# Kernel optimization log

Measured on AMD Instinct MI355X. Metric: run time of the kernel, lower is better.

Reference implementation:

```python
import jax, jax.numpy as jnp
import numpy as np

_J6 = jnp.array([[0,0,0,0,0,1],[0,0,0,0,-1,0],[0,0,0,1,0,0],
                 [0,0,1,0,0,0],[0,-1,0,0,0,0],[1,0,0,0,0,0]], dtype=jnp.float32)
_PAIRS4 = [(0,1),(0,2),(0,3),(1,2),(1,3),(2,3)]
H = 16  # n_heads

def _ln(x, g, b, eps=1e-5):
    m = jnp.mean(x, axis=-1, keepdims=True)
    v = jnp.var(x, axis=-1, keepdims=True)
    return (x - m) / jnp.sqrt(v + eps) * g + b

def _exterior(p1, p2):
    # Plucker coordinates of the line through p1,p2 in R^4 -> R^6, normalized
    parts = [p1[..., i] * p2[..., j] - p1[..., j] * p2[..., i] for i, j in _PAIRS4]
    L = jnp.stack(parts, axis=-1)
    n = jnp.linalg.norm(L, axis=-1, keepdims=True)
    return L / jnp.maximum(n, 1e-12)

def _iterated_gram_attn(x, Wqkv, bqkv, W1w, W2w, W1r, W2r, Wmv, bmv, Wmg, bmg,
                        mem_scale, iter_mix, decay_logits, Wout, bout):
    B, T, D = x.shape
    dh = D // H
    # ---- standard causal attention branch ----
    qkv = (x @ Wqkv + bqkv).reshape(B, T, 3, H, dh)
    q = jnp.transpose(qkv[:, :, 0], (0, 2, 1, 3))  # bhtd
    k = jnp.transpose(qkv[:, :, 1], (0, 2, 1, 3))
    v = jnp.transpose(qkv[:, :, 2], (0, 2, 1, 3))
    scores = jnp.einsum('bhtd,bhsd->bhts', q, k) * (dh ** -0.5)
    causal = jnp.tril(jnp.ones((T, T), dtype=bool))
    scores = jnp.where(causal, scores, -jnp.inf)
    attn = jax.nn.softmax(scores, axis=-1)  # dropout is eval-mode identity
    seq_out = jnp.einsum('bhts,bhsd->bhtd', attn, v).transpose(0, 2, 1, 3).reshape(B, T, D)
    # ---- Gram memory branch ----
    x_prev = jnp.concatenate([jnp.zeros_like(x[:, :1]), x[:, :-1]], axis=1)
    w1 = (x_prev @ W1w).reshape(B, T, H, 4)
    w2 = (x @ W2w).reshape(B, T, H, 4)
    write_lines = _exterior(w1, w2)                       # (B,T,H,6)
    r1 = (x @ W1r).reshape(B, T, H, 4)
    r2 = (x @ W2r).reshape(B, T, H, 4)
    read_lines = _exterior(r1, r2)                        # (B,T,H,6)
    Jw = jnp.einsum('bthi,ij->bhtj', write_lines, _J6)    # (B,H,T,6)
    rd = jnp.transpose(read_lines, (0, 2, 1, 3))          # (B,H,T,6)
    decays = jax.nn.sigmoid(decay_logits)                 # (H,)
    pos = jnp.arange(T, dtype=x.dtype)
    outer = Jw[..., :, None] * Jw[..., None, :]           # (B,H,T,6,6)
    dinv = (1.0 / jnp.maximum(decays, 1e-6))[:, None] ** pos[None, :]  # (H,T)
    M = jnp.cumsum(outer * dinv[None, :, :, None, None], axis=2)
    M = jnp.concatenate([jnp.zeros_like(M[:, :, :1]), M[:, :, :-1]], axis=2)  # shift: strictly past
    dfwd = decays[:, None] ** pos[None, :]
    M = M * dfwd[None, :, :, None, None]                  # (B,H,T,6,6)
    rdM = jnp.einsum('bhti,bhtij->bhtj', rd, M)
    score_M = jnp.sum(rdM * rd, axis=-1)                  # (B,H,T)
    score_M2 = jnp.sum(rdM * rdM, axis=-1)
    alpha = jax.nn.sigmoid(iter_mix[0])
    mem_score = (1 - alpha) * score_M + alpha * score_M2
    mem_val = x @ Wmv + bmv                               # (B,T,D)
    gate = jax.nn.sigmoid(x @ Wmg + bmg)                  # (B,T,H)
    gated = jax.nn.sigmoid(jnp.transpose(mem_score, (0, 2, 1)) * mem_scale[None, None, :]) * gate
    gated = jnp.mean(gated, axis=-1, keepdims=True)       # (B,T,1)
    return (seq_out + gated * mem_val) @ Wout + bout

def _block(x, ln1_g, ln1_b, Wqkv, bqkv, W1w, W2w, W1r, W2r, Wmv, bmv, Wmg, bmg,
           mem_scale, iter_mix, decay_logits, Wout, bout,
           ln2_g, ln2_b, Wfc, bfc, Wproj, bproj):
    h = _ln(x, ln1_g, ln1_b)
    x = x + _iterated_gram_attn(h, Wqkv, bqkv, W1w, W2w, W1r, W2r, Wmv, bmv,
                                Wmg, bmg, mem_scale, iter_mix, decay_logits, Wout, bout)
    h2 = _ln(x, ln2_g, ln2_b)
    mlp = jax.nn.gelu(h2 @ Wfc + bfc, approximate=False) @ Wproj + bproj
    return x + mlp

def setup_inputs() -> dict:
    key = jax.random.key(0)
    B, T, D = 2, 1024, 1024
    dff = 4 * D
    ks = jax.random.split(key, 16)
    s = 0.02
    inp = {
        'x': jax.random.normal(ks[0], (B, T, D), jnp.float32),
        'ln1_g': jnp.ones((D,), jnp.float32), 'ln1_b': jnp.zeros((D,), jnp.float32),
        'Wqkv': jax.random.normal(ks[1], (D, 3 * D), jnp.float32) * s,
        'bqkv': jnp.zeros((3 * D,), jnp.float32),
        'W1w': jax.random.normal(ks[2], (D, 4 * H), jnp.float32) * s,
        'W2w': jax.random.normal(ks[3], (D, 4 * H), jnp.float32) * s,
        'W1r': jax.random.normal(ks[4], (D, 4 * H), jnp.float32) * s,
        'W2r': jax.random.normal(ks[5], (D, 4 * H), jnp.float32) * s,
        'Wmv': jax.random.normal(ks[6], (D, D), jnp.float32) * s,
        'bmv': jnp.zeros((D,), jnp.float32),
        'Wmg': jax.random.normal(ks[7], (D, H), jnp.float32) * s,
        'bmg': jnp.zeros((H,), jnp.float32),
        'mem_scale': jnp.full((H,), 0.1, jnp.float32),
        'iter_mix': jnp.zeros((1,), jnp.float32),
        'decay_logits': jnp.full((H,), 4.6, jnp.float32) + 0.1 * jax.random.normal(ks[8], (H,), jnp.float32),
        'Wout': jax.random.normal(ks[9], (D, D), jnp.float32) * s,
        'bout': jnp.zeros((D,), jnp.float32),
        'ln2_g': jnp.ones((D,), jnp.float32), 'ln2_b': jnp.zeros((D,), jnp.float32),
        'Wfc': jax.random.normal(ks[10], (D, dff), jnp.float32) * s,
        'bfc': jnp.zeros((dff,), jnp.float32),
        'Wproj': jax.random.normal(ks[11], (dff, D), jnp.float32) * s,
        'bproj': jnp.zeros((D,), jnp.float32),
    }
    return inp

def reference(x, ln1_g, ln1_b, Wqkv, bqkv, W1w, W2w, W1r, W2r, Wmv, bmv, Wmg, bmg,
              mem_scale, iter_mix, decay_logits, Wout, bout,
              ln2_g, ln2_b, Wfc, bfc, Wproj, bproj):
    return _block(x, ln1_g, ln1_b, Wqkv, bqkv, W1w, W2w, W1r, W2r, Wmv, bmv, Wmg, bmg,
                  mem_scale, iter_mix, decay_logits, Wout, bout,
                  ln2_g, ln2_b, Wfc, bfc, Wproj, bproj)
```

## Files before the change

### kernel.cpp

```cpp
#include <hip/hip_runtime.h>
#include <hip/hip_bf16.h>
#include <math.h>

typedef float f32x4 __attribute__((ext_vector_type(4)));
typedef _Float16 f16x8 __attribute__((ext_vector_type(8)));
typedef _Float16 f16x4 __attribute__((ext_vector_type(4)));

#define TT 1024
#define DD 1024
#define QS 4608

typedef __attribute__((address_space(1))) const void gas_void;
typedef __attribute__((address_space(3))) void las_void;
static __device__ __forceinline__ void gl_lds16(const void* g, void* l) {
  __builtin_amdgcn_global_load_lds((gas_void*)g, (las_void*)l, 16, 0, 0);
}

__global__ __launch_bounds__(512) void gemm_t16(
    const _Float16* __restrict__ A, const _Float16* __restrict__ Wt,
    const float* __restrict__ bias, void* __restrict__ Cv,
    int N, int K, int act, int gx, int mode, int ktiles) {
  __shared__ __align__(16) _Float16 As[3][128 * 32];
  __shared__ __align__(16) _Float16 Bs[3][128 * 32];
  const int tid = threadIdx.x;
  const int lane = tid & 63;
  const int wid = tid >> 6;
  const int wr = wid >> 1, wc = wid & 1;
  const int g = lane >> 4, l16 = lane & 15;
  const int cpx = gridDim.x >> 3;
  const int wg = (blockIdx.x & 7) * cpx + (blockIdx.x >> 3);
  const int row0 = (wg / gx) * 128, col0 = (wg % gx) * 128;
  const int kbeg = blockIdx.y * ktiles * 32;

  f32x4 acc[2][4];
#pragma unroll
  for (int m = 0; m < 2; ++m)
#pragma unroll
    for (int n = 0; n < 4; ++n) acc[m][n] = (f32x4){0.f, 0.f, 0.f, 0.f};

  const int srow = tid >> 2;
  const int goff = ((tid & 3) ^ ((srow >> 1) & 3)) << 3;
  const _Float16* agp = A + (size_t)(row0 + srow) * K + kbeg + goff;
  const _Float16* bgp = Wt + (size_t)(col0 + srow) * K + kbeg + goff;
  const int ldst = tid * 16;

  const int prm = (l16 >> 1) & 3;

  gl_lds16(agp, (char*)As[0] + ldst);
  gl_lds16(bgp, (char*)Bs[0] + ldst);
  if (1 < ktiles) {
    gl_lds16(agp + 32, (char*)As[1] + ldst);
    gl_lds16(bgp + 32, (char*)Bs[1] + ldst);
  }

  int cs = 0, ss = 2;
  for (int kt = 0; kt < ktiles; ++kt) {
    if (kt < ktiles - 1) asm volatile("s_waitcnt vmcnt(2)" ::: "memory");
    else                 asm volatile("s_waitcnt vmcnt(0)" ::: "memory");
    __builtin_amdgcn_s_barrier();
    __builtin_amdgcn_sched_barrier(0);
    if (kt + 2 < ktiles) {
      const int kp = (kt + 2) * 32;
      gl_lds16(agp + kp, (char*)As[ss] + ldst);
      gl_lds16(bgp + kp, (char*)Bs[ss] + ldst);
    }
    f16x8 af[2], bf[4];
#pragma unroll
    for (int m = 0; m < 2; ++m) {
      const int r = wr * 32 + m * 16 + l16;
      af[m] = *(const f16x8*)(As[cs] + r * 32 + ((g ^ prm) << 3));
    }
#pragma unroll
    for (int n = 0; n < 4; ++n) {
      const int r = wc * 64 + n * 16 + l16;
      bf[n] = *(const f16x8*)(Bs[cs] + r * 32 + ((g ^ prm) << 3));
    }
#pragma unroll
    for (int m = 0; m < 2; ++m)
#pragma unroll
      for (int n = 0; n < 4; ++n)
        acc[m][n] = __builtin_amdgcn_mfma_f32_16x16x32_f16(af[m], bf[n], acc[m][n], 0, 0, 0);
    cs = (cs == 2) ? 0 : cs + 1;
    ss = (ss == 2) ? 0 : ss + 1;
  }
#pragma unroll
  for (int m = 0; m < 2; ++m) {
#pragma unroll
    for (int n = 0; n < 4; ++n) {
      const int col = col0 + wc * 64 + n * 16 + l16;
      const float bv = (mode != 2 && bias) ? bias[col] : 0.f;
#pragma unroll
      for (int rg = 0; rg < 4; ++rg) {
        const int row = row0 + wr * 32 + m * 16 + g * 4 + rg;
        const size_t off = (size_t)row * N + col;
        float v = acc[m][n][rg] + bv;
        if (act == 1) v = 0.5f * v * (1.f + erff(v * 0.70710678118654752f));
        if (mode == 2) atomicAdd(&((float*)Cv)[off], v);
        else ((_Float16*)Cv)[off] = (_Float16)v;
      }
    }
  }
}

__global__ __launch_bounds__(256) void transT(const float* __restrict__ W,
                                              _Float16* __restrict__ WT, int K, int N) {
  __shared__ float tile[64][65];
  const int n0 = blockIdx.x * 64, k0 = blockIdx.y * 64;
  const int tn = threadIdx.x & 63, tk4 = threadIdx.x >> 6;
#pragma unroll
  for (int it = 0; it < 16; ++it) {
    const int k = k0 + it * 4 + tk4;
    tile[tn][it * 4 + tk4] = W[(size_t)k * N + n0 + tn];
  }
  __syncthreads();
  const int on = threadIdx.x >> 2, ok = threadIdx.x & 3;
  f16x8 a, b;
#pragma unroll
  for (int j = 0; j < 8; ++j) {
    a[j] = (_Float16)tile[on][ok * 16 + j];
    b[j] = (_Float16)tile[on][ok * 16 + 8 + j];
  }
  _Float16* dst = WT + (size_t)(n0 + on) * K + k0 + ok * 16;
  *(f16x8*)dst = a;
  *(f16x8*)(dst + 8) = b;
}

__global__ __launch_bounds__(256) void prep_megaT(
    const float* __restrict__ Wqkv, const float* __restrict__ W1w, const float* __restrict__ W2w,
    const float* __restrict__ W1r, const float* __restrict__ W2r, const float* __restrict__ Wmg,
    const float* __restrict__ Wmv, _Float16* __restrict__ WmT) {
  __shared__ float tile[64][65];
  const int n0 = blockIdx.x * 64, k0 = blockIdx.y * 64;
  const int tn = threadIdx.x & 63, tk4 = threadIdx.x >> 6;
#pragma unroll
  for (int it = 0; it < 16; ++it) {
    const int k = k0 + it * 4 + tk4;
    const int n = n0 + tn;
    float v;
    if (n < 3072) v = Wqkv[(size_t)k * 3072 + n];
    else if (n < 3136) v = W1w[k * 64 + n - 3072];
    else if (n < 3200) v = W2w[k * 64 + n - 3136];
    else if (n < 3264) v = W1r[k * 64 + n - 3200];
    else if (n < 3328) v = W2r[k * 64 + n - 3264];
    else if (n < 3344) v = Wmg[k * 16 + n - 3328];
    else if (n < 3584) v = 0.f;
    else v = Wmv[(size_t)k * 1024 + n - 3584];
    tile[tn][it * 4 + tk4] = v;
  }
  __syncthreads();
  const int on = threadIdx.x >> 2, ok = threadIdx.x & 3;
  f16x8 a, b;
#pragma unroll
  for (int j = 0; j < 8; ++j) {
    a[j] = (_Float16)tile[on][ok * 16 + j];
    b[j] = (_Float16)tile[on][ok * 16 + 8 + j];
  }
  _Float16* dst = WmT + (size_t)(n0 + on) * 1024 + k0 + ok * 16;
  *(f16x8*)dst = a;
  *(f16x8*)(dst + 8) = b;
}

__global__ void bm_init(const float* __restrict__ bqkv, const float* __restrict__ bmg,
                        const float* __restrict__ bmv, float* __restrict__ bm) {
  const int col = blockIdx.x * 256 + threadIdx.x;
  if (col >= 4608) return;
  float b = 0.f;
  if (col < 3072) b = bqkv[col];
  else if (col >= 3328 && col < 3344) b = bmg[col - 3328];
  else if (col >= 3584) b = bmv[col - 3584];
  bm[col] = b;
}

__global__ __launch_bounds__(256) void ln16(const float* __restrict__ in,
    const float* __restrict__ gw, const float* __restrict__ bw, _Float16* __restrict__ out) {
  const int row = blockIdx.x, tid = threadIdx.x;
  const float* x = in + (size_t)row * DD;
  const float4 v = *(const float4*)(x + tid * 4);
  float s = v.x + v.y + v.z + v.w;
  float sq = v.x * v.x + v.y * v.y + v.z * v.z + v.w * v.w;
#pragma unroll
  for (int off = 32; off >= 1; off >>= 1) { s += __shfl_xor(s, off); sq += __shfl_xor(sq, off); }
  __shared__ float red[8];
  const int lane = tid & 63, wv = tid >> 6;
  if (lane == 0) { red[wv] = s; red[4 + wv] = sq; }
  __syncthreads();
  s = red[0] + red[1] + red[2] + red[3];
  sq = red[4] + red[5] + red[6] + red[7];
  const float mean = s * (1.f / 1024.f);
  const float var = sq * (1.f / 1024.f) - mean * mean;
  const float rstd = rsqrtf(var + 1e-5f);
  const float4 g4 = *(const float4*)(gw + tid * 4);
  const float4 b4 = *(const float4*)(bw + tid * 4);
  f16x4 o;
  o[0] = (_Float16)((v.x - mean) * rstd * g4.x + b4.x);
  o[1] = (_Float16)((v.y - mean) * rstd * g4.y + b4.y);
  o[2] = (_Float16)((v.z - mean) * rstd * g4.z + b4.z);
  o[3] = (_Float16)((v.w - mean) * rstd * g4.w + b4.w);
  *(f16x4*)(out + (size_t)row * DD + tid * 4) = o;
}

static __device__ __forceinline__ int swzA(int row, int k) {
  return row * 64 + ((((k >> 3) ^ row) & 7) << 3) + (k & 7);
}
static __device__ __forceinline__ int swzV(int row, int k) {
  return row * 64 + ((((k >> 3) ^ row ^ (row >> 3)) & 7) << 3) + (k & 7);
}

__global__ __launch_bounds__(256) void attn_mfma(const _Float16* __restrict__ qkv,
                                                 _Float16* __restrict__ seq_out) {
  __shared__ __align__(16) _Float16 Kl[64 * 64];
  __shared__ __align__(16) _Float16 Vt[64 * 64];
  __shared__ __align__(16) _Float16 Pl[4][16 * 64];
  const int tid = threadIdx.x, lane = tid & 63, wq = tid >> 6;
  const int g = lane >> 4, l16 = lane & 15;
  const int qt = blockIdx.x, hh = blockIdx.y, bb = blockIdx.z;
  const int nt = qt + 1;

  f16x8 qf[2];
  {
    const _Float16* qp = qkv + (size_t)(bb * TT + qt * 64 + wq * 16 + l16) * QS + hh * 64;
#pragma unroll
    for (int ks = 0; ks < 2; ++ks) {
      const f16x8 a = *(const f16x8*)(qp + ks * 32 + g * 8);
#pragma unroll
      for (int j = 0; j < 8; ++j) qf[ks][j] = (_Float16)((float)a[j] * 0.125f);
    }
  }

  f32x4 oacc[4];
#pragma unroll
  for (int n = 0; n < 4; ++n) oacc[n] = (f32x4){0.f, 0.f, 0.f, 0.f};
  float m[4] = {-INFINITY, -INFINITY, -INFINITY, -INFINITY};
  float l[4] = {0.f, 0.f, 0.f, 0.f};

  const int skey = tid >> 2, sc4 = tid & 3;

  for (int tt = 0; tt < nt; ++tt) {
    if (tt) __syncthreads();
    {
      const _Float16* kp = qkv + (size_t)(bb * TT + tt * 64 + skey) * QS + hh * 64 + 1024;
      const _Float16* vp = kp + 1024;
#pragma unroll
      for (int ii = 0; ii < 4; ++ii) {
        const int d0 = sc4 * 4 + ii * 16;
        *(f16x4*)(Kl + swzA(skey, d0)) = *(const f16x4*)(kp + d0);
        const f16x4 vv = *(const f16x4*)(vp + d0);
        Vt[swzV(d0 + 0, skey)] = vv[0];
        Vt[swzV(d0 + 1, skey)] = vv[1];
        Vt[swzV(d0 + 2, skey)] = vv[2];
        Vt[swzV(d0 + 3, skey)] = vv[3];
      }
    }
    __syncthreads();
    f32x4 s[4];
#pragma unroll
    for (int n = 0; n < 4; ++n) s[n] = (f32x4){0.f, 0.f, 0.f, 0.f};
#pragma unroll
    for (int ks = 0; ks < 2; ++ks) {
      f16x8 kf[4];
#pragma unroll
      for (int n = 0; n < 4; ++n) kf[n] = *(const f16x8*)(Kl + swzA(n * 16 + l16, ks * 32 + g * 8));
#pragma unroll
      for (int n = 0; n < 4; ++n)
        s[n] = __builtin_amdgcn_mfma_f32_16x16x32_f16(qf[ks], kf[n], s[n], 0, 0, 0);
    }
    if (tt == qt) {
      const int rloc = wq * 16 + g * 4;
#pragma unroll
      for (int n = 0; n < 4; ++n) {
        const int cloc = n * 16 + l16;
#pragma unroll
        for (int reg = 0; reg < 4; ++reg)
          if (cloc > rloc + reg) s[n][reg] = -INFINITY;
      }
    }
    float f[4];
#pragma unroll
    for (int reg = 0; reg < 4; ++reg) {
      float t = fmaxf(fmaxf(s[0][reg], s[1][reg]), fmaxf(s[2][reg], s[3][reg]));
#pragma unroll
      for (int off = 1; off < 16; off <<= 1) t = fmaxf(t, __shfl_xor(t, off));
      const float nm = fmaxf(m[reg], t);
      f[reg] = __expf(m[reg] - nm);
      m[reg] = nm;
    }
    float rs[4] = {0.f, 0.f, 0.f, 0.f};
#pragma unroll
    for (int n = 0; n < 4; ++n) {
#pragma unroll
      for (int reg = 0; reg < 4; ++reg) {
        const float p = __expf(s[n][reg] - m[reg]);
        rs[reg] += p;
        Pl[wq][swzA(g * 4 + reg, n * 16 + l16)] = (_Float16)p;
      }
    }
#pragma unroll
    for (int reg = 0; reg < 4; ++reg) {
      float t = rs[reg];
#pragma unroll
      for (int off = 1; off < 16; off <<= 1) t += __shfl_xor(t, off);
      l[reg] = l[reg] * f[reg] + t;
    }
#pragma unroll
    for (int n = 0; n < 4; ++n)
#pragma unroll
      for (int reg = 0; reg < 4; ++reg) oacc[n][reg] *= f[reg];
#pragma unroll
    for (int ks = 0; ks < 2; ++ks) {
      const f16x8 pa = *(const f16x8*)(Pl[wq] + swzA(l16, ks * 32 + g * 8));
      f16x8 vb[4];
#pragma unroll
      for (int n = 0; n < 4; ++n) vb[n] = *(const f16x8*)(Vt + swzV(n * 16 + l16, ks * 32 + g * 8));
#pragma unroll
      for (int n = 0; n < 4; ++n)
        oacc[n] = __builtin_amdgcn_mfma_f32_16x16x32_f16(pa, vb[n], oacc[n], 0, 0, 0);
    }
  }
#pragma unroll
  for (int n = 0; n < 4; ++n) {
#pragma unroll
    for (int reg = 0; reg < 4; ++reg) {
      const int r = qt * 64 + wq * 16 + g * 4 + reg;
      seq_out[(size_t)(bb * TT + r) * DD + hh * 64 + n * 16 + l16] = (_Float16)(oacc[n][reg] / l[reg]);
    }
  }
}

static __device__ __forceinline__ void ext6(const float* a, const float* b, float* L) {
  L[0] = a[0] * b[1] - a[1] * b[0];
  L[1] = a[0] * b[2] - a[2] * b[0];
  L[2] = a[0] * b[3] - a[3] * b[0];
  L[3] = a[1] * b[2] - a[2] * b[1];
  L[4] = a[1] * b[3] - a[3] * b[1];
  L[5] = a[2] * b[3] - a[3] * b[2];
  const float n = sqrtf(L[0]*L[0] + L[1]*L[1] + L[2]*L[2] + L[3]*L[3] + L[4]*L[4] + L[5]*L[5]);
  const float s = 1.f / fmaxf(n, 1e-12f);
#pragma unroll
  for (int i = 0; i < 6; ++i) L[i] *= s;
}

__global__ void lines_post(const _Float16* __restrict__ mega, float* __restrict__ jw,
                           float* __restrict__ rdv, float* __restrict__ gate) {
  const int idx = blockIdx.x * 256 + threadIdx.x;
  const int h = idx & 15;
  const int bt = idx >> 4;
  const int t = bt & 1023;
  const int b = bt >> 10;
  const _Float16* row = mega + (size_t)bt * QS + 3072;
  float w1[4] = {0.f, 0.f, 0.f, 0.f}, w2[4], r1[4], r2[4];
  if (t > 0) {
#pragma unroll
    for (int i = 0; i < 4; ++i) w1[i] = (float)row[-QS + h * 4 + i];
  }
#pragma unroll
  for (int i = 0; i < 4; ++i) {
    w2[i] = (float)row[64 + h * 4 + i];
    r1[i] = (float)row[128 + h * 4 + i];
    r2[i] = (float)row[192 + h * 4 + i];
  }
  const float gp = (float)row[256 + h];
  float wl[6], rl[6];
  ext6(w1, w2, wl);
  ext6(r1, r2, rl);
  const size_t o = ((size_t)(b * 16 + h) * 1024 + t) * 6;
  jw[o + 0] =  wl[5]; jw[o + 1] = -wl[4]; jw[o + 2] =  wl[3];
  jw[o + 3] =  wl[2]; jw[o + 4] = -wl[1]; jw[o + 5] =  wl[0];
#pragma unroll
  for (int i = 0; i < 6; ++i) rdv[o + i] = rl[i];
  gate[idx] = 1.f / (1.f + __expf(-gp));
}

static __device__ __forceinline__ int midx(int i, int j) {
  return (i <= j) ? (i * (13 - i)) / 2 + (j - i) : (j * (13 - j)) / 2 + (i - j);
}

__global__ __launch_bounds__(64) void gram_scan(const float* __restrict__ jwv,
    const float* __restrict__ rdv, const float* __restrict__ decay_logits,
    const float* __restrict__ iter_mix, float* __restrict__ mem_score) {
  const int h = blockIdx.x & 15, b = blockIdx.x >> 4;
  const int lane = threadIdx.x;
  const float decay = 1.f / (1.f + __expf(-decay_logits[h]));
  const float alpha = 1.f / (1.f + __expf(-iter_mix[0]));
  __shared__ float sd[64 * 193];
  const size_t base = (size_t)(b * 16 + h) * 1024 * 6;
  for (int it = 0; it < 96; ++it) {
    const int idx = it * 64 + lane;
    const int t = idx / 6, i = idx - 6 * t;
    const int ld = t >> 4, s = t & 15;
    sd[ld * 193 + s * 6 + i] = jwv[base + idx];
    sd[ld * 193 + 96 + s * 6 + i] = rdv[base + idx];
  }
  __syncthreads();
  const float* seg = sd + lane * 193;

  float C[21];
#pragma unroll
  for (int e = 0; e < 21; ++e) C[e] = 0.f;
  for (int s = 0; s < 16; ++s) {
    float J[6], dJ[6];
#pragma unroll
    for (int i = 0; i < 6; ++i) { J[i] = seg[s * 6 + i]; dJ[i] = decay * J[i]; }
#pragma unroll
    for (int i = 0; i < 6; ++i)
#pragma unroll
      for (int j = i; j < 6; ++j)
        C[midx(i, j)] = decay * C[midx(i, j)] + dJ[i] * J[j];
  }
  const float d2 = decay * decay, d4 = d2 * d2, d8 = d4 * d4;
  float fk = d8 * d8;
#pragma unroll
  for (int k = 0; k < 6; ++k) {
    const int off = 1 << k;
#pragma unroll
    for (int e = 0; e < 21; ++e) {
      const float u = __shfl(C[e], lane - off);
      if (lane >= off) C[e] += fk * u;
    }
    fk = fk * fk;
  }
  float M[21];
#pragma unroll
  for (int e = 0; e < 21; ++e) {
    const float u = __shfl(C[e], lane - 1);
    M[e] = (lane >= 1) ? u : 0.f;
  }
  float* msp = mem_score + (size_t)(b * 16 + h) * 1024 + lane * 16;
  for (int s = 0; s < 16; ++s) {
    float J[6], r[6];
#pragma unroll
    for (int i = 0; i < 6; ++i) { J[i] = seg[s * 6 + i]; r[i] = seg[96 + s * 6 + i]; }
    float rdM[6];
#pragma unroll
    for (int i = 0; i < 6; ++i) {
      float a = 0.f;
#pragma unroll
      for (int j = 0; j < 6; ++j) a += M[midx(i, j)] * r[j];
      rdM[i] = a;
    }
    float s1 = 0.f, s2 = 0.f;
#pragma unroll
    for (int i = 0; i < 6; ++i) { s1 += rdM[i] * r[i]; s2 += rdM[i] * rdM[i]; }
    msp[s] = (1.f - alpha) * s1 + alpha * s2;
    float dJ[6];
#pragma unroll
    for (int i = 0; i < 6; ++i) dJ[i] = decay * J[i];
#pragma unroll
    for (int i = 0; i < 6; ++i)
#pragma unroll
      for (int j = i; j < 6; ++j)
        M[midx(i, j)] = decay * M[midx(i, j)] + dJ[i] * J[j];
  }
}

__global__ __launch_bounds__(256) void combine_kernel(const _Float16* __restrict__ seq,
    const _Float16* __restrict__ mega, const float* __restrict__ ms,
    const float* __restrict__ gate, const float* __restrict__ mem_scale,
    _Float16* __restrict__ outp) {
  const int bt = blockIdx.x;
  const int b = bt >> 10, t = bt & 1023;
  __shared__ float hterm[16];
  const int tid = threadIdx.x;
  if (tid < 16) {
    const float sc = ms[(size_t)(b * 16 + tid) * 1024 + t];
    const float gt = gate[(size_t)bt * 16 + tid];
    hterm[tid] = (1.f / (1.f + __expf(-sc * mem_scale[tid]))) * gt;
  }
  __syncthreads();
  float acc = 0.f;
#pragma unroll
  for (int h = 0; h < 16; ++h) acc += hterm[h];
  const float g = acc * (1.f / 16.f);
  const f16x4 s4 = *(const f16x4*)(seq + (size_t)bt * 1024 + tid * 4);
  const f16x4 m4 = *(const f16x4*)(mega + (size_t)bt * QS + 3584 + tid * 4);
  f16x4 o;
#pragma unroll
  for (int j = 0; j < 4; ++j) o[j] = (_Float16)((float)s4[j] + g * (float)m4[j]);
  *(f16x4*)(outp + (size_t)bt * 1024 + tid * 4) = o;
}

__global__ void addb_init(const float* __restrict__ src, const float* __restrict__ bias,
                          float* __restrict__ dst) {
  const size_t i = (size_t)blockIdx.x * 256 + threadIdx.x;
  const int c4 = (int)(i & 255);
  const float4 s = ((const float4*)src)[i];
  const float4 b = ((const float4*)bias)[c4];
  float4 o;
  o.x = s.x + b.x; o.y = s.y + b.y; o.z = s.z + b.z; o.w = s.w + b.w;
  ((float4*)dst)[i] = o;
}

extern "C" void kernel_launch(void* const* d_in, const int* in_sizes, int n_in,
                              void* d_out, int out_size, void* d_ws, size_t ws_size,
                              hipStream_t stream) {
  (void)in_sizes; (void)n_in; (void)out_size; (void)ws_size;
  const float* x       = (const float*)d_in[0];
  const float* ln1_g   = (const float*)d_in[1];
  const float* ln1_b   = (const float*)d_in[2];
  const float* Wqkv    = (const float*)d_in[3];
  const float* bqkv    = (const float*)d_in[4];
  const float* W1w     = (const float*)d_in[5];
  const float* W2w     = (const float*)d_in[6];
  const float* W1r     = (const float*)d_in[7];
  const float* W2r     = (const float*)d_in[8];
  const float* Wmv     = (const float*)d_in[9];
  const float* bmv     = (const float*)d_in[10];
  const float* Wmg     = (const float*)d_in[11];
  const float* bmg     = (const float*)d_in[12];
  const float* mscale  = (const float*)d_in[13];
  const float* itermix = (const float*)d_in[14];
  const float* dlogits = (const float*)d_in[15];
  const float* Wout    = (const float*)d_in[16];
  const float* bout    = (const float*)d_in[17];
  const float* ln2_g   = (const float*)d_in[18];
  const float* ln2_b   = (const float*)d_in[19];
  const float* Wfc     = (const float*)d_in[20];
  const float* bfc     = (const float*)d_in[21];
  const float* Wproj   = (const float*)d_in[22];
  const float* bproj   = (const float*)d_in[23];
  float* out = (float*)d_out;
  float* ws = (float*)d_ws;

  const size_t M1 = 1u << 20;
  _Float16* h16    = (_Float16*)ws;
  _Float16* WmT    = (_Float16*)(ws + 1 * M1);
  float*    bm     = ws + 3407872;
  float*    jw     = ws + 3538944;
  float*    rd     = ws + 3538944 + 196608;
  float*    gate   = ws + 3538944 + 393216;
  float*    ms     = ws + 3538944 + 425984;
  float*    y      = ws + 4 * M1;
  _Float16* mega   = (_Float16*)(ws + 6 * M1);
  _Float16* fc16   = (_Float16*)(ws + 6 * M1);
  _Float16* seq16  = (_Float16*)(ws + 11010048);
  _Float16* WoutT  = (_Float16*)(ws + 12058624);
  _Float16* WfcT   = (_Float16*)(ws + 12 * M1);
  _Float16* WprojT = (_Float16*)(ws + 14 * M1);

  prep_megaT<<<dim3(72, 16), 256, 0, stream>>>(Wqkv, W1w, W2w, W1r, W2r, Wmg, Wmv, WmT);
  bm_init<<<18, 256, 0, stream>>>(bqkv, bmg, bmv, bm);
  transT<<<dim3(16, 16), 256, 0, stream>>>(Wout, WoutT, 1024, 1024);
  transT<<<dim3(64, 16), 256, 0, stream>>>(Wfc, WfcT, 1024, 4096);
  transT<<<dim3(16, 64), 256, 0, stream>>>(Wproj, WprojT, 4096, 1024);

  ln16<<<2048, 256, 0, stream>>>(x, ln1_g, ln1_b, h16);
  gemm_t16<<<576, 512, 0, stream>>>(h16, WmT, bm, mega, 4608, 1024, 0, 36, 1, 32);
  attn_mfma<<<dim3(16, 16, 2), 256, 0, stream>>>(mega, seq16);
  lines_post<<<128, 256, 0, stream>>>(mega, jw, rd, gate);
  gram_scan<<<32, 64, 0, stream>>>(jw, rd, dlogits, itermix, ms);
  combine_kernel<<<2048, 256, 0, stream>>>(seq16, mega, ms, gate, mscale, h16);
  addb_init<<<2048, 256, 0, stream>>>(x, bout, y);
  gemm_t16<<<dim3(128, 4), 512, 0, stream>>>(h16, WoutT, nullptr, y, 1024, 1024, 0, 8, 2, 8);
  ln16<<<2048, 256, 0, stream>>>(y, ln2_g, ln2_b, h16);
  gemm_t16<<<512, 512, 0, stream>>>(h16, WfcT, bfc, fc16, 4096, 1024, 1, 32, 1, 32);
  addb_init<<<2048, 256, 0, stream>>>(y, bproj, out);
  gemm_t16<<<dim3(128, 4), 512, 0, stream>>>(fc16, WprojT, nullptr, out, 1024, 4096, 0, 8, 2, 32);
}
```

Measured before the change: 251.0 us.

## Enlarge GEMM tiles to 256x128 with 64-deep K stages

The fp16 MFMA GEMM moves from 128x128x32 block tiles to 256x128x64 tiles. Each wave now holds a 4x4 accumulator grid, and each pipeline stage issues six LDS-direct loads. The aim is more arithmetic per byte loaded and fewer barrier and loop iterations per unit of K. In exchange, LDS use rises to about 144KB, which allows only one block per CU, and the grids shrink to roughly one block per CU, so tail effects and latency hiding become riskier. The row mapping now hardcodes 8 row tiles of 256, which assumes M=2048.

```diff
diff --git a/kernel.cpp b/kernel.cpp
--- a/kernel.cpp
+++ b/kernel.cpp
@@ -19,9 +19,9 @@
 __global__ __launch_bounds__(512) void gemm_t16(
     const _Float16* __restrict__ A, const _Float16* __restrict__ Wt,
     const float* __restrict__ bias, void* __restrict__ Cv,
-    int N, int K, int act, int gx, int mode, int ktiles) {
-  __shared__ __align__(16) _Float16 As[3][128 * 32];
-  __shared__ __align__(16) _Float16 Bs[3][128 * 32];
+    int N, int K, int act, int mode, int kt64) {
+  __shared__ __align__(16) _Float16 As[3][16384];
+  __shared__ __align__(16) _Float16 Bs[3][8192];
   const int tid = threadIdx.x;
   const int lane = tid & 63;
   const int wid = tid >> 6;
@@ -29,12 +29,13 @@
   const int g = lane >> 4, l16 = lane & 15;
   const int cpx = gridDim.x >> 3;
   const int wg = (blockIdx.x & 7) * cpx + (blockIdx.x >> 3);
-  const int row0 = (wg / gx) * 128, col0 = (wg % gx) * 128;
-  const int kbeg = blockIdx.y * ktiles * 32;
-
-  f32x4 acc[2][4];
-#pragma unroll
-  for (int m = 0; m < 2; ++m)
+  const int row0 = (wg & 7) * 256;
+  const int col0 = (wg >> 3) * 128;
+  const int kbeg = blockIdx.y * kt64 * 64;
+
+  f32x4 acc[4][4];
+#pragma unroll
+  for (int m = 0; m < 4; ++m)
 #pragma unroll
     for (int n = 0; n < 4; ++n) acc[m][n] = (f32x4){0.f, 0.f, 0.f, 0.f};
 
@@ -42,56 +43,64 @@
   const int goff = ((tid & 3) ^ ((srow >> 1) & 3)) << 3;
   const _Float16* agp = A + (size_t)(row0 + srow) * K + kbeg + goff;
   const _Float16* bgp = Wt + (size_t)(col0 + srow) * K + kbeg + goff;
+  const size_t arh = (size_t)128 * K;
   const int ldst = tid * 16;
 
   const int prm = (l16 >> 1) & 3;
 
-  gl_lds16(agp, (char*)As[0] + ldst);
-  gl_lds16(bgp, (char*)Bs[0] + ldst);
-  if (1 < ktiles) {
-    gl_lds16(agp + 32, (char*)As[1] + ldst);
-    gl_lds16(bgp + 32, (char*)Bs[1] + ldst);
-  }
+#define STAGE(t, slot)                                                          \
+  {                                                                             \
+    const int kp_ = (t) * 64;                                                   \
+    _Pragma("unroll")                                                           \
+    for (int s_ = 0; s_ < 2; ++s_) {                                            \
+      gl_lds16(agp + kp_ + s_ * 32,       (char*)As[slot] + s_ * 16384 + ldst); \
+      gl_lds16(agp + arh + kp_ + s_ * 32, (char*)As[slot] + s_ * 16384 + 8192 + ldst); \
+      gl_lds16(bgp + kp_ + s_ * 32,       (char*)Bs[slot] + s_ * 8192 + ldst);  \
+    }                                                                           \
+  }
+
+  STAGE(0, 0);
+  if (1 < kt64) STAGE(1, 1);
 
   int cs = 0, ss = 2;
-  for (int kt = 0; kt < ktiles; ++kt) {
-    if (kt < ktiles - 1) asm volatile("s_waitcnt vmcnt(2)" ::: "memory");
-    else                 asm volatile("s_waitcnt vmcnt(0)" ::: "memory");
+  for (int kt = 0; kt < kt64; ++kt) {
+    if (kt < kt64 - 1) asm volatile("s_waitcnt vmcnt(6)" ::: "memory");
+    else               asm volatile("s_waitcnt vmcnt(0)" ::: "memory");
     __builtin_amdgcn_s_barrier();
     __builtin_amdgcn_sched_barrier(0);
-    if (kt + 2 < ktiles) {
-      const int kp = (kt + 2) * 32;
-      gl_lds16(agp + kp, (char*)As[ss] + ldst);
-      gl_lds16(bgp + kp, (char*)Bs[ss] + ldst);
-    }
-    f16x8 af[2], bf[4];
-#pragma unroll
-    for (int m = 0; m < 2; ++m) {
-      const int r = wr * 32 + m * 16 + l16;
-      af[m] = *(const f16x8*)(As[cs] + r * 32 + ((g ^ prm) << 3));
-    }
-#pragma unroll
-    for (int n = 0; n < 4; ++n) {
-      const int r = wc * 64 + n * 16 + l16;
-      bf[n] = *(const f16x8*)(Bs[cs] + r * 32 + ((g ^ prm) << 3));
-    }
-#pragma unroll
-    for (int m = 0; m < 2; ++m)
-#pragma unroll
-      for (int n = 0; n < 4; ++n)
-        acc[m][n] = __builtin_amdgcn_mfma_f32_16x16x32_f16(af[m], bf[n], acc[m][n], 0, 0, 0);
+    if (kt + 2 < kt64) STAGE(kt + 2, ss);
+#pragma unroll
+    for (int ks = 0; ks < 2; ++ks) {
+      f16x8 af[4], bf[4];
+#pragma unroll
+      for (int m = 0; m < 4; ++m) {
+        const int r = wr * 64 + m * 16 + l16;
+        af[m] = *(const f16x8*)(As[cs] + ks * 8192 + r * 32 + ((g ^ prm) << 3));
+      }
+#pragma unroll
+      for (int n = 0; n < 4; ++n) {
+        const int c = wc * 64 + n * 16 + l16;
+        bf[n] = *(const f16x8*)(Bs[cs] + ks * 4096 + c * 32 + ((g ^ prm) << 3));
+      }
+#pragma unroll
+      for (int m = 0; m < 4; ++m)
+#pragma unroll
+        for (int n = 0; n < 4; ++n)
+          acc[m][n] = __builtin_amdgcn_mfma_f32_16x16x32_f16(af[m], bf[n], acc[m][n], 0, 0, 0);
+    }
     cs = (cs == 2) ? 0 : cs + 1;
     ss = (ss == 2) ? 0 : ss + 1;
   }
-#pragma unroll
-  for (int m = 0; m < 2; ++m) {
+#undef STAGE
+#pragma unroll
+  for (int m = 0; m < 4; ++m) {
 #pragma unroll
     for (int n = 0; n < 4; ++n) {
       const int col = col0 + wc * 64 + n * 16 + l16;
       const float bv = (mode != 2 && bias) ? bias[col] : 0.f;
 #pragma unroll
       for (int rg = 0; rg < 4; ++rg) {
-        const int row = row0 + wr * 32 + m * 16 + g * 4 + rg;
+        const int row = row0 + wr * 64 + m * 16 + g * 4 + rg;
         const size_t off = (size_t)row * N + col;
         float v = acc[m][n][rg] + bv;
         if (act == 1) v = 0.5f * v * (1.f + erff(v * 0.70710678118654752f));
@@ -543,15 +552,15 @@
   transT<<<dim3(16, 64), 256, 0, stream>>>(Wproj, WprojT, 4096, 1024);
 
   ln16<<<2048, 256, 0, stream>>>(x, ln1_g, ln1_b, h16);
-  gemm_t16<<<576, 512, 0, stream>>>(h16, WmT, bm, mega, 4608, 1024, 0, 36, 1, 32);
+  gemm_t16<<<288, 512, 0, stream>>>(h16, WmT, bm, mega, 4608, 1024, 0, 1, 16);
   attn_mfma<<<dim3(16, 16, 2), 256, 0, stream>>>(mega, seq16);
   lines_post<<<128, 256, 0, stream>>>(mega, jw, rd, gate);
   gram_scan<<<32, 64, 0, stream>>>(jw, rd, dlogits, itermix, ms);
   combine_kernel<<<2048, 256, 0, stream>>>(seq16, mega, ms, gate, mscale, h16);
   addb_init<<<2048, 256, 0, stream>>>(x, bout, y);
-  gemm_t16<<<dim3(128, 4), 512, 0, stream>>>(h16, WoutT, nullptr, y, 1024, 1024, 0, 8, 2, 8);
+  gemm_t16<<<dim3(64, 4), 512, 0, stream>>>(h16, WoutT, nullptr, y, 1024, 1024, 0, 2, 4);
   ln16<<<2048, 256, 0, stream>>>(y, ln2_g, ln2_b, h16);
-  gemm_t16<<<512, 512, 0, stream>>>(h16, WfcT, bfc, fc16, 4096, 1024, 1, 32, 1, 32);
+  gemm_t16<<<256, 512, 0, stream>>>(h16, WfcT, bfc, fc16, 4096, 1024, 1, 1, 16);
   addb_init<<<2048, 256, 0, stream>>>(y, bproj, out);
-  gemm_t16<<<dim3(128, 4), 512, 0, stream>>>(fc16, WprojT, nullptr, out, 1024, 4096, 0, 8, 2, 32);
-}
+  gemm_t16<<<dim3(64, 4), 512, 0, stream>>>(fc16, WprojT, nullptr, out, 1024, 4096, 0, 2, 16);
+}
```

After: 287.1 us. 1.14x slower.

## Shrink GEMM tiles to 64x128 with 256 threads and double-buffered LDS

Applied to the files above, without the earlier changes.

The fp16 MFMA GEMM now uses 64x128 output tiles, 256 threads and two LDS stages instead of 128x128 tiles, 512 threads and a three-stage pipeline. The row index is hardcoded to 32 row tiles, and the grids double to give more workgroups and smaller LDS footprints, which may raise occupancy. In exchange, each B tile is reused across fewer rows, adding global traffic, and the shallower prefetch plus an extra barrier per k-step can expose more load latency.

```diff
diff --git a/kernel.cpp b/kernel.cpp
--- a/kernel.cpp
+++ b/kernel.cpp
@@ -16,12 +16,12 @@
   __builtin_amdgcn_global_load_lds((gas_void*)g, (las_void*)l, 16, 0, 0);
 }
 
-__global__ __launch_bounds__(512) void gemm_t16(
+__global__ __launch_bounds__(256) void gemm_t16(
     const _Float16* __restrict__ A, const _Float16* __restrict__ Wt,
     const float* __restrict__ bias, void* __restrict__ Cv,
-    int N, int K, int act, int gx, int mode, int ktiles) {
-  __shared__ __align__(16) _Float16 As[3][128 * 32];
-  __shared__ __align__(16) _Float16 Bs[3][128 * 32];
+    int N, int K, int act, int mode, int nt) {
+  __shared__ __align__(16) _Float16 As[2][2048];
+  __shared__ __align__(16) _Float16 Bs[2][4096];
   const int tid = threadIdx.x;
   const int lane = tid & 63;
   const int wid = tid >> 6;
@@ -29,8 +29,9 @@
   const int g = lane >> 4, l16 = lane & 15;
   const int cpx = gridDim.x >> 3;
   const int wg = (blockIdx.x & 7) * cpx + (blockIdx.x >> 3);
-  const int row0 = (wg / gx) * 128, col0 = (wg % gx) * 128;
-  const int kbeg = blockIdx.y * ktiles * 32;
+  const int row0 = (wg & 31) * 64;
+  const int col0 = (wg >> 5) * 128;
+  const int kbeg = blockIdx.y * nt * 32;
 
   f32x4 acc[2][4];
 #pragma unroll
@@ -41,48 +42,49 @@
   const int srow = tid >> 2;
   const int goff = ((tid & 3) ^ ((srow >> 1) & 3)) << 3;
   const _Float16* agp = A + (size_t)(row0 + srow) * K + kbeg + goff;
-  const _Float16* bgp = Wt + (size_t)(col0 + srow) * K + kbeg + goff;
+  const _Float16* bgp0 = Wt + (size_t)(col0 + srow) * K + kbeg + goff;
+  const _Float16* bgp1 = Wt + (size_t)(col0 + 64 + srow) * K + kbeg + goff;
   const int ldst = tid * 16;
 
   const int prm = (l16 >> 1) & 3;
 
-  gl_lds16(agp, (char*)As[0] + ldst);
-  gl_lds16(bgp, (char*)Bs[0] + ldst);
-  if (1 < ktiles) {
-    gl_lds16(agp + 32, (char*)As[1] + ldst);
-    gl_lds16(bgp + 32, (char*)Bs[1] + ldst);
-  }
-
-  int cs = 0, ss = 2;
-  for (int kt = 0; kt < ktiles; ++kt) {
-    if (kt < ktiles - 1) asm volatile("s_waitcnt vmcnt(2)" ::: "memory");
-    else                 asm volatile("s_waitcnt vmcnt(0)" ::: "memory");
+#define STAGE(T, B) {                                        \
+    const int kp_ = (T) * 32;                                \
+    gl_lds16(agp + kp_, (char*)As[B] + ldst);                \
+    gl_lds16(bgp0 + kp_, (char*)Bs[B] + ldst);               \
+    gl_lds16(bgp1 + kp_, (char*)Bs[B] + 4096 + ldst); }
+
+  STAGE(0, 0);
+  for (int kt = 0; kt < nt; ++kt) {
+    if (kt + 1 < nt) {
+      STAGE(kt + 1, (kt + 1) & 1);
+      asm volatile("s_waitcnt vmcnt(3)" ::: "memory");
+    } else {
+      asm volatile("s_waitcnt vmcnt(0)" ::: "memory");
+    }
     __builtin_amdgcn_s_barrier();
     __builtin_amdgcn_sched_barrier(0);
-    if (kt + 2 < ktiles) {
-      const int kp = (kt + 2) * 32;
-      gl_lds16(agp + kp, (char*)As[ss] + ldst);
-      gl_lds16(bgp + kp, (char*)Bs[ss] + ldst);
-    }
+    const int cb = kt & 1;
     f16x8 af[2], bf[4];
 #pragma unroll
     for (int m = 0; m < 2; ++m) {
       const int r = wr * 32 + m * 16 + l16;
-      af[m] = *(const f16x8*)(As[cs] + r * 32 + ((g ^ prm) << 3));
+      af[m] = *(const f16x8*)(As[cb] + r * 32 + ((g ^ prm) << 3));
     }
 #pragma unroll
     for (int n = 0; n < 4; ++n) {
-      const int r = wc * 64 + n * 16 + l16;
-      bf[n] = *(const f16x8*)(Bs[cs] + r * 32 + ((g ^ prm) << 3));
+      const int c = wc * 64 + n * 16 + l16;
+      bf[n] = *(const f16x8*)(Bs[cb] + c * 32 + ((g ^ prm) << 3));
     }
 #pragma unroll
     for (int m = 0; m < 2; ++m)
 #pragma unroll
       for (int n = 0; n < 4; ++n)
         acc[m][n] = __builtin_amdgcn_mfma_f32_16x16x32_f16(af[m], bf[n], acc[m][n], 0, 0, 0);
-    cs = (cs == 2) ? 0 : cs + 1;
-    ss = (ss == 2) ? 0 : ss + 1;
-  }
+    __builtin_amdgcn_s_barrier();
+  }
+#undef STAGE
+
 #pragma unroll
   for (int m = 0; m < 2; ++m) {
 #pragma unroll
@@ -543,15 +545,15 @@
   transT<<<dim3(16, 64), 256, 0, stream>>>(Wproj, WprojT, 4096, 1024);
 
   ln16<<<2048, 256, 0, stream>>>(x, ln1_g, ln1_b, h16);
-  gemm_t16<<<576, 512, 0, stream>>>(h16, WmT, bm, mega, 4608, 1024, 0, 36, 1, 32);
+  gemm_t16<<<1152, 256, 0, stream>>>(h16, WmT, bm, mega, 4608, 1024, 0, 1, 32);
   attn_mfma<<<dim3(16, 16, 2), 256, 0, stream>>>(mega, seq16);
   lines_post<<<128, 256, 0, stream>>>(mega, jw, rd, gate);
   gram_scan<<<32, 64, 0, stream>>>(jw, rd, dlogits, itermix, ms);
   combine_kernel<<<2048, 256, 0, stream>>>(seq16, mega, ms, gate, mscale, h16);
   addb_init<<<2048, 256, 0, stream>>>(x, bout, y);
-  gemm_t16<<<dim3(128, 4), 512, 0, stream>>>(h16, WoutT, nullptr, y, 1024, 1024, 0, 8, 2, 8);
+  gemm_t16<<<dim3(256, 4), 256, 0, stream>>>(h16, WoutT, nullptr, y, 1024, 1024, 0, 2, 8);
   ln16<<<2048, 256, 0, stream>>>(y, ln2_g, ln2_b, h16);
-  gemm_t16<<<512, 512, 0, stream>>>(h16, WfcT, bfc, fc16, 4096, 1024, 1, 32, 1, 32);
+  gemm_t16<<<1024, 256, 0, stream>>>(h16, WfcT, bfc, fc16, 4096, 1024, 1, 1, 32);
   addb_init<<<2048, 256, 0, stream>>>(y, bproj, out);
-  gemm_t16<<<dim3(128, 4), 512, 0, stream>>>(fc16, WprojT, nullptr, out, 1024, 4096, 0, 8, 2, 32);
-}
+  gemm_t16<<<dim3(256, 4), 256, 0, stream>>>(fc16, WprojT, nullptr, out, 1024, 4096, 0, 2, 32);
+}
```

Measured after the change: 264.3 us. 1.05x slower.
